# Optimization experiments

Measured on AMD Instinct MI355X. Metric: run time of the kernel, lower is better.

The kernel has to match this reference:

```python
import jax, jax.numpy as jnp
import numpy as np

UNITS = 256
FEAT = 256
NUM_BLOCKS = 4  # start_gru + 2 middle blocks + end_gru
BATCH, T = 128, 384


def _gru_layer(x, kernel, rkernel, bias, return_sequences):
    """Keras GRU (reset_after=True, tanh/sigmoid), zero initial state.
    x: [B,T,D]; kernel: [D,3U]; rkernel: [U,3U]; bias: [2,3U] (input, recurrent).
    Gate order z, r, h as in Keras.
    """
    u = rkernel.shape[0]
    # Precompute input projections for all timesteps (one big GEMM)
    xp = jnp.einsum('btd,dg->btg', x, kernel) + bias[0]  # [B,T,3U]

    def step(h, xt):
        rh = h @ rkernel + bias[1]                 # [B,3U]
        mz, mr, mh = jnp.split(xt, 3, axis=-1)
        rz, rr, rhh = jnp.split(rh, 3, axis=-1)
        z = jax.nn.sigmoid(mz + rz)
        r = jax.nn.sigmoid(mr + rr)
        hh = jnp.tanh(mh + r * rhh)                # reset_after: r applied after recurrent matmul
        h_new = z * h + (1.0 - z) * hh
        return h_new, h_new

    h0 = jnp.zeros((x.shape[0], u), dtype=x.dtype)
    hT, hs = jax.lax.scan(step, h0, jnp.swapaxes(xp, 0, 1))  # scan over time
    return jnp.swapaxes(hs, 0, 1) if return_sequences else hT


def setup_inputs() -> dict:
    key = jax.random.key(0)
    ks = jax.random.split(key, 8)
    s_in = 1.0 / np.sqrt(FEAT)
    s_u = 1.0 / np.sqrt(UNITS)
    x = jax.random.normal(ks[0], (BATCH, T, FEAT), dtype=jnp.float32)
    # first layer params
    k0 = jax.random.normal(ks[1], (FEAT, 3 * UNITS), dtype=jnp.float32) * s_in
    rk0 = jax.random.normal(ks[2], (UNITS, 3 * UNITS), dtype=jnp.float32) * s_u
    b0 = jnp.zeros((2, 3 * UNITS), dtype=jnp.float32)
    # remaining NUM_BLOCKS-1 layers, stacked along leading axis
    L = NUM_BLOCKS - 1
    kern = jax.random.normal(ks[3], (L, UNITS, 3 * UNITS), dtype=jnp.float32) * s_u
    rkern = jax.random.normal(ks[4], (L, UNITS, 3 * UNITS), dtype=jnp.float32) * s_u
    bias = jnp.zeros((L, 2, 3 * UNITS), dtype=jnp.float32)
    return {"x": x, "k0": k0, "rk0": rk0, "b0": b0,
            "kern": kern, "rkern": rkern, "bias": bias}


def reference(x, k0, rk0, b0, kern, rkern, bias):
    # start_gru: return_sequences=True
    h = _gru_layer(x, k0, rk0, b0, return_sequences=True)
    L = kern.shape[0]
    # middle blocks return_sequences=True, last (end_gru) returns final state only
    for i in range(L):
        last = (i == L - 1)
        h = _gru_layer(h, kern[i], rkern[i], bias[i], return_sequences=not last)
    return h  # [B, UNITS]
```

## Files before the change

### kernel.cpp

```cpp
#include <hip/hip_runtime.h>
#include <hip/hip_fp16.h>


#define LAYERS 4
#define TSTEPS 384
#define NCH    8
#define WPL    (48 * 16 * 64 * 8)
#define TILE_STRIDE (16 * 64 * 8)
#define RING   16
#define SLOT_ULL (16 * 128)
#define GRP_ULL  (RING * SLOT_ULL)

typedef _Float16 half8 __attribute__((ext_vector_type(8)));
typedef float    f32x4 __attribute__((ext_vector_type(4)));
typedef unsigned uint4v __attribute__((ext_vector_type(4)));
typedef unsigned long long ull;

#define WP_OFF   0
#define BP_OFF   (LAYERS * WPL * 2)
#define FLAG_OFF (BP_OFF + LAYERS * 1024 * 4)
#define FLAG_BYTES 4096
#define HBUF_OFF (4 * 1024 * 1024)

#define SCOPE __HIP_MEMORY_SCOPE_AGENT

__global__ void repack_kernel(const float* __restrict__ k0, const float* __restrict__ rk0,
                              const float* __restrict__ b0, const float* __restrict__ kern,
                              const float* __restrict__ rkern, const float* __restrict__ bias,
                              _Float16* __restrict__ Wp, float* __restrict__ Bp)
{
    int idx = blockIdx.x * 256 + threadIdx.x;
    const int total_w = LAYERS * WPL;
    if (idx < total_w) {
        int l = idx / WPL;
        int r = idx - l * WPL;
        int j    = r & 7;
        int lane = (r >> 3) & 63;
        int kt   = (r >> 9) & 15;
        int tile = r >> 13;
        int n = tile * 16 + (lane & 15);
        int k = kt * 32 + (lane >> 4) * 8 + j;
        float v;
        if (l == 0) {
            v = (k < 256) ? k0[(size_t)k * 768 + n] : rk0[(size_t)(k - 256) * 768 + n];
        } else {
            const float* kk = kern  + (size_t)(l - 1) * 256 * 768;
            const float* rk = rkern + (size_t)(l - 1) * 256 * 768;
            v = (k < 256) ? kk[(size_t)k * 768 + n] : rk[(size_t)(k - 256) * 768 + n];
        }
        Wp[idx] = (_Float16)v;
    } else {
        int ib = idx - total_w;
        if (ib < LAYERS * 1024) {
            int l = ib >> 10;
            int i = ib & 1023;
            const float* bs = (l == 0) ? b0 : (bias + (size_t)(l - 1) * 2 * 768);
            float v;
            if (i < 512)      v = bs[i] + bs[768 + i];
            else if (i < 768) v = bs[512 + (i - 512)];
            else              v = bs[768 + 512 + (i - 768)];
            Bp[l * 1024 + i] = v;
        }
    }
}

__launch_bounds__(384, 1)
__global__ void gru_kernel(const float* __restrict__ x,
                           const _Float16* __restrict__ Wp,
                           const float* __restrict__ Bp,
                           ull* __restrict__ hbuf,
                           unsigned int* __restrict__ flags,
                           float* __restrict__ out)
{
    __shared__ _Float16 Af[2][16 * 512];
    __shared__ float    Sc[8][16][17];

    const int tid  = threadIdx.x;
    const int lane = tid & 63;
    const int w    = tid >> 6;
    const int lo16 = lane & 15;
    const int q    = lane >> 4;

    const int s = blockIdx.x & 7;
    const int c = (blockIdx.x >> 3) & 7;
    const int l = blockIdx.x >> 6;
    const int b0row = c * 16;

    const int tile = (w >> 1) * 16 + 2 * s + (w & 1);
    half8 bfrag[16];
    {
        const _Float16* wb = Wp + (size_t)l * WPL + (size_t)tile * TILE_STRIDE;
#pragma unroll
        for (int kt = 0; kt < 16; ++kt)
            bfrag[kt] = *(const half8*)(wb + ((size_t)kt * 64 + lane) * 8);
    }

    const int grow = tid >> 4;
    const int g16  = tid & 15;
    const int gup  = g16 * 2;
    const int ktx  = g16 >> 1;
    const int qq   = (g16 & 1) * 2;
    const int xoff0 = ((ktx * 64) + qq * 16 + grow) * 8;
    const int xoff1 = ((ktx * 64) + (qq + 1) * 16 + grow) * 8;
    const int hoff0 = (((8 + ktx) * 64) + qq * 16 + grow) * 8;
    const int hoff1 = (((8 + ktx) * 64) + (qq + 1) * 16 + grow) * 8;

    float bz[2] = {0,0}, br[2] = {0,0}, bi[2] = {0,0}, bh[2] = {0,0};
    float hprev[2] = {0.f, 0.f};
    if (tid < 256) {
        const float* bp = Bp + l * 1024;
        int ug = s * 32 + gup;
        bz[0] = bp[ug];       bz[1] = bp[ug + 1];
        br[0] = bp[256 + ug]; br[1] = bp[256 + ug + 1];
        bi[0] = bp[512 + ug]; bi[1] = bp[512 + ug + 1];
        bh[0] = bp[768 + ug]; bh[1] = bp[768 + ug + 1];
    }

    unsigned int* fl_own_g = flags + (l * NCH + c) * 16;
    unsigned int* fl_dn_g  = flags + ((l < 3 ? l + 1 : 0) * NCH + c) * 16;
    unsigned int* my_flag  = fl_own_g + s;

    ull*       hb_own = hbuf + (size_t)(l * NCH + c) * GRP_ULL;
    const ull* hb_up  = hbuf + (size_t)((l > 0 ? l - 1 : 0) * NCH + c) * GRP_ULL;

    auto wait_group = [&](const unsigned int* base, unsigned need) {
        for (;;) {
            unsigned v = 0xFFFFFFFFu;
            if (lane < 8)
                v = __hip_atomic_load(base + lane, __ATOMIC_RELAXED, SCOPE);
            if (__all((int)(v >= need))) return;
            __builtin_amdgcn_s_sleep(1);
        }
    };

    auto stage_x = [&](int t, _Float16* An) {
        if (l == 0) {
            const float* sp = x + ((size_t)(b0row + grow) * TSTEPS + t) * 256 + gup * 8;
            f32x4 a0 = *(const f32x4*)sp,      a1 = *(const f32x4*)(sp + 4);
            f32x4 a2 = *(const f32x4*)(sp + 8), a3 = *(const f32x4*)(sp + 12);
            half8 h0, h1;
            h0[0]=(_Float16)a0[0]; h0[1]=(_Float16)a0[1]; h0[2]=(_Float16)a0[2]; h0[3]=(_Float16)a0[3];
            h0[4]=(_Float16)a1[0]; h0[5]=(_Float16)a1[1]; h0[6]=(_Float16)a1[2]; h0[7]=(_Float16)a1[3];
            h1[0]=(_Float16)a2[0]; h1[1]=(_Float16)a2[1]; h1[2]=(_Float16)a2[2]; h1[3]=(_Float16)a2[3];
            h1[4]=(_Float16)a3[0]; h1[5]=(_Float16)a3[1]; h1[6]=(_Float16)a3[2]; h1[7]=(_Float16)a3[3];
            *(half8*)(An + xoff0) = h0;
            *(half8*)(An + xoff1) = h1;
        } else {
            const ull* spx = hb_up + (size_t)(t & (RING - 1)) * SLOT_ULL + grow * 128 + g16 * 8;
            const unsigned tg = (unsigned)(t + 1);
            ull vx[8];
#pragma unroll
            for (int j = 0; j < 8; ++j)
                vx[j] = __hip_atomic_load(spx + j, __ATOMIC_RELAXED, SCOPE);
            for (;;) {
                bool ok = true;
#pragma unroll
                for (int j = 0; j < 8; ++j)
                    if ((unsigned)(vx[j] >> 32) != tg) {
                        vx[j] = __hip_atomic_load(spx + j, __ATOMIC_RELAXED, SCOPE);
                        ok = false;
                    }
                if (ok) break;
                __builtin_amdgcn_s_sleep(1);
            }
            uint4v w0, w1;
            w0[0]=(unsigned)vx[0]; w0[1]=(unsigned)vx[1]; w0[2]=(unsigned)vx[2]; w0[3]=(unsigned)vx[3];
            w1[0]=(unsigned)vx[4]; w1[1]=(unsigned)vx[5]; w1[2]=(unsigned)vx[6]; w1[3]=(unsigned)vx[7];
            *(uint4v*)(An + xoff0) = w0;
            *(uint4v*)(An + xoff1) = w1;
        }
    };

    if (tid < 256) {
        stage_x(0, Af[0]);
        uint4v z = {0u, 0u, 0u, 0u};
        *(uint4v*)(Af[0] + hoff0) = z;
        *(uint4v*)(Af[0] + hoff1) = z;
    }

    ull vh[8];

    for (int t = 0; t < TSTEPS; ++t) {
        _Float16* A  = Af[t & 1];
        _Float16* An = Af[(t + 1) & 1];

        if (t > 0 && tid < 256) {
            const ull* sph = hb_own + (size_t)((t - 1) & (RING - 1)) * SLOT_ULL + grow * 128 + g16 * 8;
            const unsigned tg = (unsigned)t;
            for (;;) {
                bool ok = true;
#pragma unroll
                for (int j = 0; j < 8; ++j)
                    if ((unsigned)(vh[j] >> 32) != tg) {
                        vh[j] = __hip_atomic_load(sph + j, __ATOMIC_RELAXED, SCOPE);
                        ok = false;
                    }
                if (ok) break;
            }
            uint4v w0, w1;
            w0[0]=(unsigned)vh[0]; w0[1]=(unsigned)vh[1]; w0[2]=(unsigned)vh[2]; w0[3]=(unsigned)vh[3];
            w1[0]=(unsigned)vh[4]; w1[1]=(unsigned)vh[5]; w1[2]=(unsigned)vh[6]; w1[3]=(unsigned)vh[7];
            *(uint4v*)(A + hoff0) = w0;
            *(uint4v*)(A + hoff1) = w1;
        }
        __syncthreads();

        f32x4 acc0 = {0,0,0,0}, acc1 = {0,0,0,0};
#pragma unroll
        for (int kt = 0; kt < 16; ++kt) {
            half8 a = *(const half8*)(A + ((kt * 64) + lane) * 8);
            if (w < 4 || kt < 8)
                acc0 = __builtin_amdgcn_mfma_f32_16x16x32_f16(a, bfrag[kt], acc0, 0, 0, 0);
            else
                acc1 = __builtin_amdgcn_mfma_f32_16x16x32_f16(a, bfrag[kt], acc1, 0, 0, 0);
        }
#pragma unroll
        for (int r = 0; r < 4; ++r) Sc[w][q * 4 + r][lo16] = acc0[r];
        if (w >= 4) {
#pragma unroll
            for (int r = 0; r < 4; ++r) Sc[w + 2][q * 4 + r][lo16] = acc1[r];
        }
        __syncthreads();

        if (l < 3 && t >= RING) wait_group(fl_dn_g, (unsigned)(t - RING + 1));

        if (tid < 256) {
            float hn[2];
#pragma unroll
            for (int j = 0; j < 2; ++j) {
                int u   = gup + j;
                int ut  = u >> 4;
                int col = u & 15;
                float zp = Sc[ut][grow][col]     + bz[j];
                float rp = Sc[2 + ut][grow][col] + br[j];
                float ip = Sc[4 + ut][grow][col] + bi[j];
                float hp = Sc[6 + ut][grow][col] + bh[j];
                float z  = 1.f / (1.f + __expf(-zp));
                float rr = 1.f / (1.f + __expf(-rp));
                float pre = ip + rr * hp;
                float e  = __expf(2.f * pre);
                float th = 1.f - 2.f / (e + 1.f);
                hn[j] = z * hprev[j] + (1.f - z) * th;
                hprev[j] = hn[j];
            }
            union { _Float16 h[2]; unsigned u32; } pk;
            pk.h[0] = (_Float16)hn[0];
            pk.h[1] = (_Float16)hn[1];
            ull word = ((ull)(unsigned)(t + 1) << 32) | (ull)pk.u32;
            __hip_atomic_store(hb_own + (size_t)(t & (RING - 1)) * SLOT_ULL + grow * 128 + s * 16 + g16,
                               word, __ATOMIC_RELAXED, SCOPE);
            if (l == 3 && t == TSTEPS - 1) {
                float* op = out + (size_t)(b0row + grow) * 256 + s * 32 + gup;
                op[0] = hn[0];
                op[1] = hn[1];
            }
        }

        if (t + 1 < TSTEPS && tid < 256) {
            stage_x(t + 1, An);
            const ull* sph = hb_own + (size_t)(t & (RING - 1)) * SLOT_ULL + grow * 128 + g16 * 8;
#pragma unroll
            for (int j = 0; j < 8; ++j)
                vh[j] = __hip_atomic_load(sph + j, __ATOMIC_RELAXED, SCOPE);
        }
        __syncthreads();

        if (tid == 0)
            __hip_atomic_store(my_flag, (unsigned)(t + 1), __ATOMIC_RELAXED, SCOPE);
    }
}

extern "C" void kernel_launch(void* const* d_in, const int* in_sizes, int n_in,
                              void* d_out, int out_size, void* d_ws, size_t ws_size,
                              hipStream_t stream)
{
    const float* x     = (const float*)d_in[0];
    const float* k0    = (const float*)d_in[1];
    const float* rk0   = (const float*)d_in[2];
    const float* b0    = (const float*)d_in[3];
    const float* kern  = (const float*)d_in[4];
    const float* rkern = (const float*)d_in[5];
    const float* bias  = (const float*)d_in[6];
    float* out = (float*)d_out;

    char* ws = (char*)d_ws;
    _Float16*     Wp    = (_Float16*)(ws + WP_OFF);
    float*        Bp    = (float*)(ws + BP_OFF);
    unsigned int* flags = (unsigned int*)(ws + FLAG_OFF);
    ull*          hbuf  = (ull*)(ws + HBUF_OFF);

    hipMemsetAsync(flags, 0, FLAG_BYTES, stream);

    const int total = LAYERS * WPL + LAYERS * 1024;
    repack_kernel<<<(total + 255) / 256, 256, 0, stream>>>(k0, rk0, b0, kern, rkern, bias, Wp, Bp);

    gru_kernel<<<LAYERS * NCH * 8, 384, 0, stream>>>(x, Wp, Bp, hbuf, flags, out);
}
```

Before: 1.660 ms.

## Split each layer-chunk over two 512-thread blocks with per-wave fused gate MFMAs

The work split changes from 8 blocks per (layer, batch chunk) to 2 blocks of 8 waves. Each wave holds z, r and h weight fragments for 16 units and computes all gates in registers, which removes the shared-memory scratch exchange. The block writes its new hidden state directly into the next A buffer and exchanges only the partner half through global memory, so fewer blocks take part in each cross-block handshake. In exchange, each wave issues more MFMAs per step and holds more weight registers, which reduces parallelism across CUs.

```diff
diff --git a/kernel.cpp b/kernel.cpp
--- a/kernel.cpp
+++ b/kernel.cpp
@@ -23,6 +23,7 @@
 #define HBUF_OFF (4 * 1024 * 1024)
 
 #define SCOPE __HIP_MEMORY_SCOPE_AGENT
+#define MFMA __builtin_amdgcn_mfma_f32_16x16x32_f16
 
 __global__ void repack_kernel(const float* __restrict__ k0, const float* __restrict__ rk0,
                               const float* __restrict__ b0, const float* __restrict__ kern,
@@ -64,7 +65,7 @@
     }
 }
 
-__launch_bounds__(384, 1)
+__launch_bounds__(512, 2)
 __global__ void gru_kernel(const float* __restrict__ x,
                            const _Float16* __restrict__ Wp,
                            const float* __restrict__ Bp,
@@ -73,7 +74,6 @@
                            float* __restrict__ out)
 {
     __shared__ _Float16 Af[2][16 * 512];
-    __shared__ float    Sc[8][16][17];
 
     const int tid  = threadIdx.x;
     const int lane = tid & 63;
@@ -81,18 +81,30 @@
     const int lo16 = lane & 15;
     const int q    = lane >> 4;
 
-    const int s = blockIdx.x & 7;
-    const int c = (blockIdx.x >> 3) & 7;
-    const int l = blockIdx.x >> 6;
+    const int e = blockIdx.x & 1;
+    const int c = (blockIdx.x >> 1) & 7;
+    const int l = blockIdx.x >> 4;
+    const int g = l * NCH + c;
     const int b0row = c * 16;
 
-    const int tile = (w >> 1) * 16 + 2 * s + (w & 1);
-    half8 bfrag[16];
+    half8 bzf[16], brf[16], bhf[16];
     {
-        const _Float16* wb = Wp + (size_t)l * WPL + (size_t)tile * TILE_STRIDE;
-#pragma unroll
-        for (int kt = 0; kt < 16; ++kt)
-            bfrag[kt] = *(const half8*)(wb + ((size_t)kt * 64 + lane) * 8);
+        const _Float16* wb = Wp + (size_t)l * WPL;
+        const int zt = 8 * e + w, rt = 16 + 8 * e + w, ht = 32 + 8 * e + w;
+#pragma unroll
+        for (int kt = 0; kt < 16; ++kt) {
+            const size_t o = ((size_t)kt * 64 + lane) * 8;
+            bzf[kt] = *(const half8*)(wb + (size_t)zt * TILE_STRIDE + o);
+            brf[kt] = *(const half8*)(wb + (size_t)rt * TILE_STRIDE + o);
+            bhf[kt] = *(const half8*)(wb + (size_t)ht * TILE_STRIDE + o);
+        }
+    }
+
+    const int u0 = 128 * e + 16 * w + lo16;
+    float Bz, Br, Bi, Bh;
+    {
+        const float* bp = Bp + l * 1024;
+        Bz = bp[u0]; Br = bp[256 + u0]; Bi = bp[512 + u0]; Bh = bp[768 + u0];
     }
 
     const int grow = tid >> 4;
@@ -102,32 +114,30 @@
     const int qq   = (g16 & 1) * 2;
     const int xoff0 = ((ktx * 64) + qq * 16 + grow) * 8;
     const int xoff1 = ((ktx * 64) + (qq + 1) * 16 + grow) * 8;
-    const int hoff0 = (((8 + ktx) * 64) + qq * 16 + grow) * 8;
-    const int hoff1 = (((8 + ktx) * 64) + (qq + 1) * 16 + grow) * 8;
-
-    float bz[2] = {0,0}, br[2] = {0,0}, bi[2] = {0,0}, bh[2] = {0,0};
-    float hprev[2] = {0.f, 0.f};
-    if (tid < 256) {
-        const float* bp = Bp + l * 1024;
-        int ug = s * 32 + gup;
-        bz[0] = bp[ug];       bz[1] = bp[ug + 1];
-        br[0] = bp[256 + ug]; br[1] = bp[256 + ug + 1];
-        bi[0] = bp[512 + ug]; bi[1] = bp[512 + ug + 1];
-        bh[0] = bp[768 + ug]; bh[1] = bp[768 + ug + 1];
-    }
-
-    unsigned int* fl_own_g = flags + (l * NCH + c) * 16;
-    unsigned int* fl_dn_g  = flags + ((l < 3 ? l + 1 : 0) * NCH + c) * 16;
-    unsigned int* my_flag  = fl_own_g + s;
-
-    ull*       hb_own = hbuf + (size_t)(l * NCH + c) * GRP_ULL;
-    const ull* hb_up  = hbuf + (size_t)((l > 0 ? l - 1 : 0) * NCH + c) * GRP_ULL;
-
-    auto wait_group = [&](const unsigned int* base, unsigned need) {
+
+    const int rr = tid >> 5;
+    const int k5 = tid & 31;
+    const int uown = 128 * e + 4 * k5;
+    const int wown = 64 * e + 2 * k5;
+    const int upar = 128 * (1 - e) + 4 * k5;
+    const int wpar = 64 * (1 - e) + 2 * k5;
+    auto hoff = [](int u, int r) {
+        return ((8 + (u >> 5)) * 64 + ((u & 31) >> 3) * 16 + r) * 8 + (u & 7);
+    };
+    const int po = hoff(uown, rr);
+    const int so = hoff(upar, rr);
+
+    unsigned int* my_flag = flags + g * 2 + e;
+    unsigned int* fl_dn   = flags + (g + NCH) * 2;
+
+    ull*       hb_own = hbuf + (size_t)g * GRP_ULL;
+    const ull* hb_up  = hbuf + (size_t)(l > 0 ? g - NCH : g) * GRP_ULL;
+
+    auto wait_dn = [&](unsigned need) {
         for (;;) {
             unsigned v = 0xFFFFFFFFu;
-            if (lane < 8)
-                v = __hip_atomic_load(base + lane, __ATOMIC_RELAXED, SCOPE);
+            if (lane < 2)
+                v = __hip_atomic_load(fl_dn + lane, __ATOMIC_RELAXED, SCOPE);
             if (__all((int)(v >= need))) return;
             __builtin_amdgcn_s_sleep(1);
         }
@@ -136,7 +146,7 @@
     auto stage_x = [&](int t, _Float16* An) {
         if (l == 0) {
             const float* sp = x + ((size_t)(b0row + grow) * TSTEPS + t) * 256 + gup * 8;
-            f32x4 a0 = *(const f32x4*)sp,      a1 = *(const f32x4*)(sp + 4);
+            f32x4 a0 = *(const f32x4*)sp,       a1 = *(const f32x4*)(sp + 4);
             f32x4 a2 = *(const f32x4*)(sp + 8), a3 = *(const f32x4*)(sp + 12);
             half8 h0, h1;
             h0[0]=(_Float16)a0[0]; h0[1]=(_Float16)a0[1]; h0[2]=(_Float16)a0[2]; h0[3]=(_Float16)a0[3];
@@ -171,97 +181,87 @@
         }
     };
 
-    if (tid < 256) {
-        stage_x(0, Af[0]);
+    if (tid < 256) stage_x(0, Af[0]);
+    {
         uint4v z = {0u, 0u, 0u, 0u};
-        *(uint4v*)(Af[0] + hoff0) = z;
-        *(uint4v*)(Af[0] + hoff1) = z;
-    }
-
-    ull vh[8];
+        *(uint4v*)(Af[0] + ((8 + (tid >> 6)) * 64 + (tid & 63)) * 8) = z;
+    }
+
+    ull vh0, vh1;
+    float hpv[4] = {0.f, 0.f, 0.f, 0.f};
 
     for (int t = 0; t < TSTEPS; ++t) {
         _Float16* A  = Af[t & 1];
         _Float16* An = Af[(t + 1) & 1];
 
-        if (t > 0 && tid < 256) {
-            const ull* sph = hb_own + (size_t)((t - 1) & (RING - 1)) * SLOT_ULL + grow * 128 + g16 * 8;
+        if (t > 0) {
+            const ull* sp = hb_own + (size_t)((t - 1) & (RING - 1)) * SLOT_ULL + rr * 128 + wpar;
             const unsigned tg = (unsigned)t;
             for (;;) {
                 bool ok = true;
-#pragma unroll
-                for (int j = 0; j < 8; ++j)
-                    if ((unsigned)(vh[j] >> 32) != tg) {
-                        vh[j] = __hip_atomic_load(sph + j, __ATOMIC_RELAXED, SCOPE);
-                        ok = false;
-                    }
+                if ((unsigned)(vh0 >> 32) != tg) {
+                    vh0 = __hip_atomic_load(sp + 0, __ATOMIC_RELAXED, SCOPE); ok = false;
+                }
+                if ((unsigned)(vh1 >> 32) != tg) {
+                    vh1 = __hip_atomic_load(sp + 1, __ATOMIC_RELAXED, SCOPE); ok = false;
+                }
                 if (ok) break;
             }
-            uint4v w0, w1;
-            w0[0]=(unsigned)vh[0]; w0[1]=(unsigned)vh[1]; w0[2]=(unsigned)vh[2]; w0[3]=(unsigned)vh[3];
-            w1[0]=(unsigned)vh[4]; w1[1]=(unsigned)vh[5]; w1[2]=(unsigned)vh[6]; w1[3]=(unsigned)vh[7];
-            *(uint4v*)(A + hoff0) = w0;
-            *(uint4v*)(A + hoff1) = w1;
+            ull hv = ((ull)(unsigned)vh1 << 32) | (ull)(unsigned)vh0;
+            *(ull*)(A + so) = hv;
         }
         __syncthreads();
 
-        f32x4 acc0 = {0,0,0,0}, acc1 = {0,0,0,0};
+        f32x4 az = {0,0,0,0}, ar = {0,0,0,0}, ai = {0,0,0,0}, ah = {0,0,0,0};
 #pragma unroll
         for (int kt = 0; kt < 16; ++kt) {
             half8 a = *(const half8*)(A + ((kt * 64) + lane) * 8);
-            if (w < 4 || kt < 8)
-                acc0 = __builtin_amdgcn_mfma_f32_16x16x32_f16(a, bfrag[kt], acc0, 0, 0, 0);
-            else
-                acc1 = __builtin_amdgcn_mfma_f32_16x16x32_f16(a, bfrag[kt], acc1, 0, 0, 0);
-        }
-#pragma unroll
-        for (int r = 0; r < 4; ++r) Sc[w][q * 4 + r][lo16] = acc0[r];
-        if (w >= 4) {
-#pragma unroll
-            for (int r = 0; r < 4; ++r) Sc[w + 2][q * 4 + r][lo16] = acc1[r];
+            az = MFMA(a, bzf[kt], az, 0, 0, 0);
+            ar = MFMA(a, brf[kt], ar, 0, 0, 0);
+            if (kt < 8) ai = MFMA(a, bhf[kt], ai, 0, 0, 0);
+            else        ah = MFMA(a, bhf[kt], ah, 0, 0, 0);
+        }
+
+        float hn[4];
+#pragma unroll
+        for (int j = 0; j < 4; ++j) {
+            float zp = az[j] + Bz;
+            float rp = ar[j] + Br;
+            float ip = ai[j] + Bi;
+            float hp = ah[j] + Bh;
+            float z  = 1.f / (1.f + __expf(-zp));
+            float r  = 1.f / (1.f + __expf(-rp));
+            float pre = ip + r * hp;
+            float ex  = __expf(2.f * pre);
+            float th  = 1.f - 2.f / (ex + 1.f);
+            hn[j] = z * hpv[j] + (1.f - z) * th;
+            hpv[j] = hn[j];
+        }
+#pragma unroll
+        for (int j = 0; j < 4; ++j)
+            An[hoff(u0, 4 * q + j)] = (_Float16)hn[j];
+        if (l == 3 && t == TSTEPS - 1) {
+#pragma unroll
+            for (int j = 0; j < 4; ++j)
+                out[(size_t)(b0row + 4 * q + j) * 256 + u0] = hn[j];
         }
         __syncthreads();
 
-        if (l < 3 && t >= RING) wait_group(fl_dn_g, (unsigned)(t - RING + 1));
-
-        if (tid < 256) {
-            float hn[2];
-#pragma unroll
-            for (int j = 0; j < 2; ++j) {
-                int u   = gup + j;
-                int ut  = u >> 4;
-                int col = u & 15;
-                float zp = Sc[ut][grow][col]     + bz[j];
-                float rp = Sc[2 + ut][grow][col] + br[j];
-                float ip = Sc[4 + ut][grow][col] + bi[j];
-                float hp = Sc[6 + ut][grow][col] + bh[j];
-                float z  = 1.f / (1.f + __expf(-zp));
-                float rr = 1.f / (1.f + __expf(-rp));
-                float pre = ip + rr * hp;
-                float e  = __expf(2.f * pre);
-                float th = 1.f - 2.f / (e + 1.f);
-                hn[j] = z * hprev[j] + (1.f - z) * th;
-                hprev[j] = hn[j];
-            }
-            union { _Float16 h[2]; unsigned u32; } pk;
-            pk.h[0] = (_Float16)hn[0];
-            pk.h[1] = (_Float16)hn[1];
-            ull word = ((ull)(unsigned)(t + 1) << 32) | (ull)pk.u32;
-            __hip_atomic_store(hb_own + (size_t)(t & (RING - 1)) * SLOT_ULL + grow * 128 + s * 16 + g16,
-                               word, __ATOMIC_RELAXED, SCOPE);
-            if (l == 3 && t == TSTEPS - 1) {
-                float* op = out + (size_t)(b0row + grow) * 256 + s * 32 + gup;
-                op[0] = hn[0];
-                op[1] = hn[1];
-            }
-        }
-
-        if (t + 1 < TSTEPS && tid < 256) {
-            stage_x(t + 1, An);
-            const ull* sph = hb_own + (size_t)(t & (RING - 1)) * SLOT_ULL + grow * 128 + g16 * 8;
-#pragma unroll
-            for (int j = 0; j < 8; ++j)
-                vh[j] = __hip_atomic_load(sph + j, __ATOMIC_RELAXED, SCOPE);
+        if (l < 3 && t >= RING) wait_dn((unsigned)(t - RING + 1));
+
+        {
+            ull hv = *(const ull*)(An + po);
+            ull* dst = hb_own + (size_t)(t & (RING - 1)) * SLOT_ULL + rr * 128 + wown;
+            const ull tg = ((ull)(unsigned)(t + 1)) << 32;
+            __hip_atomic_store(dst + 0, tg | (ull)(unsigned)hv,         __ATOMIC_RELAXED, SCOPE);
+            __hip_atomic_store(dst + 1, tg | (ull)(unsigned)(hv >> 32), __ATOMIC_RELAXED, SCOPE);
+        }
+
+        if (t + 1 < TSTEPS) {
+            if (tid < 256) stage_x(t + 1, An);
+            const ull* sp = hb_own + (size_t)(t & (RING - 1)) * SLOT_ULL + rr * 128 + wpar;
+            vh0 = __hip_atomic_load(sp + 0, __ATOMIC_RELAXED, SCOPE);
+            vh1 = __hip_atomic_load(sp + 1, __ATOMIC_RELAXED, SCOPE);
         }
         __syncthreads();
 
@@ -294,5 +294,5 @@
     const int total = LAYERS * WPL + LAYERS * 1024;
     repack_kernel<<<(total + 255) / 256, 256, 0, stream>>>(k0, rk0, b0, kern, rkern, bias, Wp, Bp);
 
-    gru_kernel<<<LAYERS * NCH * 8, 384, 0, stream>>>(x, Wp, Bp, hbuf, flags, out);
+    gru_kernel<<<LAYERS * NCH * 2, 512, 0, stream>>>(x, Wp, Bp, hbuf, flags, out);
 }
```

New measurement: 1.864 ms. 12.3% more time.
